# Kernel tuning notes

Measured on AMD Instinct MI355X. Metric: run time of the kernel, lower is better.

Reference implementation:

```python
import jax, jax.numpy as jnp
import numpy as np

N = 8192
IN_F = 256
OUT_F = 256


def setup_inputs() -> dict:
    key = jax.random.key(0)
    k_v, k_adj, k1, k2, k3, kb = jax.random.split(key, 6)
    stdv = 1.0 / np.sqrt(OUT_F)
    V = jax.random.normal(k_v, (N, IN_F), dtype=jnp.float32)
    adj = jax.random.randint(k_adj, (N, N), 0, 4, dtype=jnp.int32)
    w1 = jax.random.uniform(k1, (IN_F, OUT_F), jnp.float32, -stdv, stdv)
    w2 = jax.random.uniform(k2, (IN_F, OUT_F), jnp.float32, -stdv, stdv)
    w3 = jax.random.uniform(k3, (IN_F, OUT_F), jnp.float32, -stdv, stdv)
    bias = jax.random.uniform(kb, (OUT_F,), jnp.float32, -stdv, stdv)
    return {"V": V, "adj": adj, "w1": w1, "w2": w2, "w3": w3, "bias": bias}


def reference(V, adj, w1, w2, w3, bias):
    # typed relational GCN: for each edge type k in {1,2,3},
    # aggregate (adj==k) @ (V @ wk), then sum and add bias
    o1 = jnp.matmul((adj == 1).astype(jnp.float32), jnp.matmul(V, w1))
    o2 = jnp.matmul((adj == 2).astype(jnp.float32), jnp.matmul(V, w2))
    o3 = jnp.matmul((adj == 3).astype(jnp.float32), jnp.matmul(V, w3))
    return o1 + o2 + o3 + bias
```

## Files before the change

kernel.cpp:

```cpp
#include <hip/hip_runtime.h>

typedef __attribute__((ext_vector_type(4))) float f32x4;
typedef __attribute__((ext_vector_type(16))) float f32x16;
typedef __attribute__((ext_vector_type(4))) unsigned short u16x4;
typedef __attribute__((ext_vector_type(4))) int i32x4;
typedef __attribute__((ext_vector_type(8))) __bf16 bf16x8;

union FragAB {
  u16x4 u[2];
  i32x4 v;
  bf16x8 f;
};

static __device__ __forceinline__ unsigned short f2bf(float x) {
  union { float f; unsigned u; } v;
  v.f = x;
  unsigned r = v.u + 0x7FFFu + ((v.u >> 16) & 1u);
  return (unsigned short)(r >> 16);
}

#define NN 8192

__global__ __launch_bounds__(256) void k_bias(const float* __restrict__ bias,
                                              float* __restrict__ out) {
  out[(size_t)blockIdx.x * 256 + threadIdx.x] = bias[threadIdx.x];
}

__global__ __launch_bounds__(256) void k_transform(
    const float* __restrict__ V, const float* __restrict__ w1,
    const float* __restrict__ w2, const float* __restrict__ w3,
    unsigned short* __restrict__ Bp) {
  int bx = blockIdx.x;
  int rb = bx & 63;
  int nb = bx >> 6;
  const float* W = (nb < 4) ? w1 : (nb < 8) ? w2 : w3;
  int nc0 = (nb & 3) * 64;
  int tid = threadIdx.x;
  int lane = tid & 63;
  int wv = tid >> 6;
  int wm = wv >> 1, wn = wv & 1;
  int q = lane >> 4, l16 = lane & 15;

  __shared__ unsigned short tA[128][36];
  __shared__ unsigned short tB[64][36];

  f32x4 acc[4][2];
#pragma unroll
  for (int i = 0; i < 4; i++)
#pragma unroll
    for (int j = 0; j < 2; j++) acc[i][j] = (f32x4)0.0f;

  for (int kk = 0; kk < 256; kk += 32) {
    {
      int r = tid >> 1, c0 = (tid & 1) * 16;
      const float* src = V + (size_t)(rb * 128 + r) * 256 + kk + c0;
      f32x4 f0 = *(const f32x4*)(src + 0);
      f32x4 f1 = *(const f32x4*)(src + 4);
      f32x4 f2 = *(const f32x4*)(src + 8);
      f32x4 f3 = *(const f32x4*)(src + 12);
      unsigned short* d = &tA[r][c0];
      d[0] = f2bf(f0.x);  d[1] = f2bf(f0.y);  d[2] = f2bf(f0.z);  d[3] = f2bf(f0.w);
      d[4] = f2bf(f1.x);  d[5] = f2bf(f1.y);  d[6] = f2bf(f1.z);  d[7] = f2bf(f1.w);
      d[8] = f2bf(f2.x);  d[9] = f2bf(f2.y);  d[10] = f2bf(f2.z); d[11] = f2bf(f2.w);
      d[12] = f2bf(f3.x); d[13] = f2bf(f3.y); d[14] = f2bf(f3.z); d[15] = f2bf(f3.w);
    }
    {
      int r = tid >> 3, c0 = (tid & 7) * 8;
      const float* src = W + (size_t)(kk + r) * 256 + nc0 + c0;
      f32x4 g0 = *(const f32x4*)(src);
      f32x4 g1 = *(const f32x4*)(src + 4);
      tB[c0 + 0][r] = f2bf(g0.x); tB[c0 + 1][r] = f2bf(g0.y);
      tB[c0 + 2][r] = f2bf(g0.z); tB[c0 + 3][r] = f2bf(g0.w);
      tB[c0 + 4][r] = f2bf(g1.x); tB[c0 + 5][r] = f2bf(g1.y);
      tB[c0 + 6][r] = f2bf(g1.z); tB[c0 + 7][r] = f2bf(g1.w);
    }
    __syncthreads();
    FragAB af[4], bf[2];
#pragma unroll
    for (int mt = 0; mt < 4; mt++) {
      const unsigned short* p = &tA[wm * 64 + mt * 16 + l16][q * 8];
      af[mt].u[0] = *(const u16x4*)p;
      af[mt].u[1] = *(const u16x4*)(p + 4);
    }
#pragma unroll
    for (int nt = 0; nt < 2; nt++) {
      const unsigned short* p = &tB[wn * 32 + nt * 16 + l16][q * 8];
      bf[nt].u[0] = *(const u16x4*)p;
      bf[nt].u[1] = *(const u16x4*)(p + 4);
    }
#pragma unroll
    for (int mt = 0; mt < 4; mt++)
#pragma unroll
      for (int nt = 0; nt < 2; nt++)
        acc[mt][nt] = __builtin_amdgcn_mfma_f32_16x16x32_bf16(
            af[mt].f, bf[nt].f, acc[mt][nt], 0, 0, 0);
    __syncthreads();
  }
  int ty = nb >> 2;
#pragma unroll
  for (int mt = 0; mt < 4; mt++)
#pragma unroll
    for (int nt = 0; nt < 2; nt++) {
      int n = (nb & 3) * 64 + wn * 32 + nt * 16 + l16;
      int j0 = rb * 128 + wm * 64 + mt * 16 + q * 4;
      u16x4 hv;
      hv.x = f2bf(acc[mt][nt].x);
      hv.y = f2bf(acc[mt][nt].y);
      hv.z = f2bf(acc[mt][nt].z);
      hv.w = f2bf(acc[mt][nt].w);
      size_t idx = (size_t)ty * 2097152 + (size_t)(j0 >> 4) * 4096 + n * 16 + (j0 & 15);
      *(u16x4*)(Bp + idx) = hv;
    }
}

__global__ __launch_bounds__(512) void k_agg(const int* __restrict__ adj,
                                             const unsigned short* __restrict__ Bp,
                                             float* __restrict__ out) {
  int bx = blockIdx.x;
  int ks = bx & 3, rb = bx >> 2;
  int tid = threadIdx.x, lane = tid & 63;
  int wv = tid >> 6;
  int wm = wv >> 2, wn = wv & 3;
  int q = lane >> 5, l32 = lane & 31;

  __shared__ unsigned short msk[3][128][36];

  f32x16 acc[2][2];
  acc[0][0] = (f32x16)0.0f;
  acc[0][1] = (f32x16)0.0f;
  acc[1][0] = (f32x16)0.0f;
  acc[1][1] = (f32x16)0.0f;

  int sr = tid >> 2, scg = tid & 3;
  const int* ap = adj + (size_t)(rb * 128 + sr) * NN + ks * 2048 + scg * 8;

  const unsigned short* bb[3][2];
#pragma unroll
  for (int ty = 0; ty < 3; ty++)
#pragma unroll
    for (int nt = 0; nt < 2; nt++) {
      int n = wn * 64 + nt * 32 + l32;
      bb[ty][nt] = Bp + (size_t)ty * 2097152 + (size_t)ks * 524288 + n * 16 + q * 8;
    }

  i32x4 a0 = *(const i32x4*)ap;
  i32x4 a1 = *(const i32x4*)(ap + 4);

  for (int step = 0; step < 64; step++) {
    {
      int av[8] = {a0.x, a0.y, a0.z, a0.w, a1.x, a1.y, a1.z, a1.w};
#pragma unroll
      for (int ty = 0; ty < 3; ty++) {
        u16x4 lo, hi;
        lo.x = (av[0] == ty + 1) ? 0x3F80 : 0;
        lo.y = (av[1] == ty + 1) ? 0x3F80 : 0;
        lo.z = (av[2] == ty + 1) ? 0x3F80 : 0;
        lo.w = (av[3] == ty + 1) ? 0x3F80 : 0;
        hi.x = (av[4] == ty + 1) ? 0x3F80 : 0;
        hi.y = (av[5] == ty + 1) ? 0x3F80 : 0;
        hi.z = (av[6] == ty + 1) ? 0x3F80 : 0;
        hi.w = (av[7] == ty + 1) ? 0x3F80 : 0;
        unsigned short* d = &msk[ty][sr][scg * 8];
        *(u16x4*)d = lo;
        *(u16x4*)(d + 4) = hi;
      }
    }
    __syncthreads();
    if (step < 63) {
      ap += 32;
      a0 = *(const i32x4*)ap;
      a1 = *(const i32x4*)(ap + 4);
    }
    int boff = step * 8192;
#pragma unroll
    for (int kh = 0; kh < 2; kh++)
#pragma unroll
      for (int ty = 0; ty < 3; ty++) {
        FragAB af[2], bf[2];
#pragma unroll
        for (int mt = 0; mt < 2; mt++) {
          const unsigned short* p =
              &msk[ty][wm * 64 + mt * 32 + l32][kh * 16 + q * 8];
          af[mt].u[0] = *(const u16x4*)p;
          af[mt].u[1] = *(const u16x4*)(p + 4);
        }
#pragma unroll
        for (int nt = 0; nt < 2; nt++) {
          const unsigned short* p = bb[ty][nt] + boff + kh * 4096;
          bf[nt].v = *(const i32x4*)p;
        }
        acc[0][0] = __builtin_amdgcn_mfma_f32_32x32x16_bf16(af[0].f, bf[0].f,
                                                            acc[0][0], 0, 0, 0);
        acc[0][1] = __builtin_amdgcn_mfma_f32_32x32x16_bf16(af[0].f, bf[1].f,
                                                            acc[0][1], 0, 0, 0);
        acc[1][0] = __builtin_amdgcn_mfma_f32_32x32x16_bf16(af[1].f, bf[0].f,
                                                            acc[1][0], 0, 0, 0);
        acc[1][1] = __builtin_amdgcn_mfma_f32_32x32x16_bf16(af[1].f, bf[1].f,
                                                            acc[1][1], 0, 0, 0);
      }
    __syncthreads();
  }
#pragma unroll
  for (int mt = 0; mt < 2; mt++)
#pragma unroll
    for (int nt = 0; nt < 2; nt++) {
      int colbase = wn * 64 + nt * 32 + l32;
      int rowb = rb * 128 + wm * 64 + mt * 32 + 4 * q;
#pragma unroll
      for (int r = 0; r < 16; r++) {
        int row = rowb + (r & 3) + 8 * (r >> 2);
        atomicAdd(out + (size_t)row * 256 + colbase, acc[mt][nt][r]);
      }
    }
}

extern "C" void kernel_launch(void* const* d_in, const int* in_sizes, int n_in,
                              void* d_out, int out_size, void* d_ws,
                              size_t ws_size, hipStream_t stream) {
  const float* V = (const float*)d_in[0];
  const int* adj = (const int*)d_in[1];
  const float* w1 = (const float*)d_in[2];
  const float* w2 = (const float*)d_in[3];
  const float* w3 = (const float*)d_in[4];
  const float* bias = (const float*)d_in[5];
  float* out = (float*)d_out;
  unsigned short* Bp = (unsigned short*)d_ws;

  k_bias<<<dim3(NN), dim3(256), 0, stream>>>(bias, out);
  k_transform<<<dim3(768), dim3(256), 0, stream>>>(V, w1, w2, w3, Bp);
  k_agg<<<dim3(256), dim3(512), 0, stream>>>(adj, Bp, out);
}
```

Measured before the change: 577.5 us.

## Double-buffer adjacency masks and retile aggregation into smaller blocks with more K-splits

Result: faster. 488.3 us (-15.4%).

```diff
diff --git a/kernel.cpp b/kernel.cpp
--- a/kernel.cpp
+++ b/kernel.cpp
@@ -113,17 +113,16 @@
     }
 }
 
-__global__ __launch_bounds__(512) void k_agg(const int* __restrict__ adj,
+__global__ __launch_bounds__(256) void k_agg(const int* __restrict__ adj,
                                              const unsigned short* __restrict__ Bp,
                                              float* __restrict__ out) {
   int bx = blockIdx.x;
-  int ks = bx & 3, rb = bx >> 2;
+  int ks = bx & 7, rb = bx >> 3;
   int tid = threadIdx.x, lane = tid & 63;
-  int wv = tid >> 6;
-  int wm = wv >> 2, wn = wv & 3;
+  int wn = tid >> 6;
   int q = lane >> 5, l32 = lane & 31;
 
-  __shared__ unsigned short msk[3][128][36];
+  __shared__ unsigned short msk[2][3][64][36];
 
   f32x16 acc[2][2];
   acc[0][0] = (f32x16)0.0f;
@@ -132,7 +131,7 @@
   acc[1][1] = (f32x16)0.0f;
 
   int sr = tid >> 2, scg = tid & 3;
-  const int* ap = adj + (size_t)(rb * 128 + sr) * NN + ks * 2048 + scg * 8;
+  const int* ap = adj + (size_t)(rb * 64 + sr) * NN + ks * 1024 + scg * 8;
 
   const unsigned short* bb[3][2];
 #pragma unroll
@@ -140,14 +139,71 @@
 #pragma unroll
     for (int nt = 0; nt < 2; nt++) {
       int n = wn * 64 + nt * 32 + l32;
-      bb[ty][nt] = Bp + (size_t)ty * 2097152 + (size_t)ks * 524288 + n * 16 + q * 8;
+      bb[ty][nt] = Bp + (size_t)ty * 2097152 + (size_t)ks * 262144 + n * 16 + q * 8;
     }
 
   i32x4 a0 = *(const i32x4*)ap;
   i32x4 a1 = *(const i32x4*)(ap + 4);
-
-  for (int step = 0; step < 64; step++) {
-    {
+  ap += 32;
+  {
+    int av[8] = {a0.x, a0.y, a0.z, a0.w, a1.x, a1.y, a1.z, a1.w};
+#pragma unroll
+    for (int ty = 0; ty < 3; ty++) {
+      u16x4 lo, hi;
+      lo.x = (av[0] == ty + 1) ? 0x3F80 : 0;
+      lo.y = (av[1] == ty + 1) ? 0x3F80 : 0;
+      lo.z = (av[2] == ty + 1) ? 0x3F80 : 0;
+      lo.w = (av[3] == ty + 1) ? 0x3F80 : 0;
+      hi.x = (av[4] == ty + 1) ? 0x3F80 : 0;
+      hi.y = (av[5] == ty + 1) ? 0x3F80 : 0;
+      hi.z = (av[6] == ty + 1) ? 0x3F80 : 0;
+      hi.w = (av[7] == ty + 1) ? 0x3F80 : 0;
+      unsigned short* d = &msk[0][ty][sr][scg * 8];
+      *(u16x4*)d = lo;
+      *(u16x4*)(d + 4) = hi;
+    }
+  }
+  a0 = *(const i32x4*)ap;
+  a1 = *(const i32x4*)(ap + 4);
+  ap += 32;
+  __syncthreads();
+
+  for (int step = 0; step < 32; step++) {
+    int buf = step & 1;
+    FragAB bv[2][3][2];
+    size_t soff = (size_t)step * 8192;
+#pragma unroll
+    for (int kh = 0; kh < 2; kh++)
+#pragma unroll
+      for (int ty = 0; ty < 3; ty++)
+#pragma unroll
+        for (int nt = 0; nt < 2; nt++)
+          bv[kh][ty][nt].v = *(const i32x4*)(bb[ty][nt] + soff + kh * 4096);
+    FragAB af[2][3][2];
+#pragma unroll
+    for (int kh = 0; kh < 2; kh++)
+#pragma unroll
+      for (int ty = 0; ty < 3; ty++)
+#pragma unroll
+        for (int mt = 0; mt < 2; mt++) {
+          const unsigned short* p = &msk[buf][ty][mt * 32 + l32][kh * 16 + q * 8];
+          af[kh][ty][mt].u[0] = *(const u16x4*)p;
+          af[kh][ty][mt].u[1] = *(const u16x4*)(p + 4);
+        }
+#pragma unroll
+    for (int kh = 0; kh < 2; kh++)
+#pragma unroll
+      for (int ty = 0; ty < 3; ty++) {
+        acc[0][0] = __builtin_amdgcn_mfma_f32_32x32x16_bf16(
+            af[kh][ty][0].f, bv[kh][ty][0].f, acc[0][0], 0, 0, 0);
+        acc[0][1] = __builtin_amdgcn_mfma_f32_32x32x16_bf16(
+            af[kh][ty][0].f, bv[kh][ty][1].f, acc[0][1], 0, 0, 0);
+        acc[1][0] = __builtin_amdgcn_mfma_f32_32x32x16_bf16(
+            af[kh][ty][1].f, bv[kh][ty][0].f, acc[1][0], 0, 0, 0);
+        acc[1][1] = __builtin_amdgcn_mfma_f32_32x32x16_bf16(
+            af[kh][ty][1].f, bv[kh][ty][1].f, acc[1][1], 0, 0, 0);
+      }
+    if (step < 31) {
       int av[8] = {a0.x, a0.y, a0.z, a0.w, a1.x, a1.y, a1.z, a1.w};
 #pragma unroll
       for (int ty = 0; ty < 3; ty++) {
@@ -160,44 +216,16 @@
         hi.y = (av[5] == ty + 1) ? 0x3F80 : 0;
         hi.z = (av[6] == ty + 1) ? 0x3F80 : 0;
         hi.w = (av[7] == ty + 1) ? 0x3F80 : 0;
-        unsigned short* d = &msk[ty][sr][scg * 8];
+        unsigned short* d = &msk[buf ^ 1][ty][sr][scg * 8];
         *(u16x4*)d = lo;
         *(u16x4*)(d + 4) = hi;
       }
-    }
-    __syncthreads();
-    if (step < 63) {
-      ap += 32;
-      a0 = *(const i32x4*)ap;
-      a1 = *(const i32x4*)(ap + 4);
-    }
-    int boff = step * 8192;
-#pragma unroll
-    for (int kh = 0; kh < 2; kh++)
-#pragma unroll
-      for (int ty = 0; ty < 3; ty++) {
-        FragAB af[2], bf[2];
-#pragma unroll
-        for (int mt = 0; mt < 2; mt++) {
-          const unsigned short* p =
-              &msk[ty][wm * 64 + mt * 32 + l32][kh * 16 + q * 8];
-          af[mt].u[0] = *(const u16x4*)p;
-          af[mt].u[1] = *(const u16x4*)(p + 4);
-        }
-#pragma unroll
-        for (int nt = 0; nt < 2; nt++) {
-          const unsigned short* p = bb[ty][nt] + boff + kh * 4096;
-          bf[nt].v = *(const i32x4*)p;
-        }
-        acc[0][0] = __builtin_amdgcn_mfma_f32_32x32x16_bf16(af[0].f, bf[0].f,
-                                                            acc[0][0], 0, 0, 0);
-        acc[0][1] = __builtin_amdgcn_mfma_f32_32x32x16_bf16(af[0].f, bf[1].f,
-                                                            acc[0][1], 0, 0, 0);
-        acc[1][0] = __builtin_amdgcn_mfma_f32_32x32x16_bf16(af[1].f, bf[0].f,
-                                                            acc[1][0], 0, 0, 0);
-        acc[1][1] = __builtin_amdgcn_mfma_f32_32x32x16_bf16(af[1].f, bf[1].f,
-                                                            acc[1][1], 0, 0, 0);
-      }
+      if (step < 30) {
+        a0 = *(const i32x4*)ap;
+        a1 = *(const i32x4*)(ap + 4);
+        ap += 32;
+      }
+    }
     __syncthreads();
   }
 #pragma unroll
@@ -205,7 +233,7 @@
 #pragma unroll
     for (int nt = 0; nt < 2; nt++) {
       int colbase = wn * 64 + nt * 32 + l32;
-      int rowb = rb * 128 + wm * 64 + mt * 32 + 4 * q;
+      int rowb = rb * 64 + mt * 32 + 4 * q;
 #pragma unroll
       for (int r = 0; r < 16; r++) {
         int row = rowb + (r & 3) + 8 * (r >> 2);
@@ -228,5 +256,5 @@
 
   k_bias<<<dim3(NN), dim3(256), 0, stream>>>(bias, out);
   k_transform<<<dim3(768), dim3(256), 0, stream>>>(V, w1, w2, w3, Bp);
-  k_agg<<<dim3(256), dim3(512), 0, stream>>>(adj, Bp, out);
-}
+  k_agg<<<dim3(1024), dim3(256), 0, stream>>>(adj, Bp, out);
+}
```

## Restructure aggregation kernel with per-wave private adj staging and no block barriers

Applied to the files above, without the earlier changes.

Result: faster. 490.0 us (-15.2%).

```diff
diff --git a/kernel.cpp b/kernel.cpp
--- a/kernel.cpp
+++ b/kernel.cpp
@@ -113,17 +113,17 @@
     }
 }
 
-__global__ __launch_bounds__(512) void k_agg(const int* __restrict__ adj,
+__global__ __launch_bounds__(256) void k_agg(const int* __restrict__ adj,
                                              const unsigned short* __restrict__ Bp,
                                              float* __restrict__ out) {
   int bx = blockIdx.x;
   int ks = bx & 3, rb = bx >> 2;
   int tid = threadIdx.x, lane = tid & 63;
   int wv = tid >> 6;
-  int wm = wv >> 2, wn = wv & 3;
   int q = lane >> 5, l32 = lane & 31;
 
-  __shared__ unsigned short msk[3][128][36];
+  __shared__ __align__(16) int smem[16384];
+  int* wbase = smem + wv * 4096;
 
   f32x16 acc[2][2];
   acc[0][0] = (f32x16)0.0f;
@@ -131,81 +131,90 @@
   acc[1][0] = (f32x16)0.0f;
   acc[1][1] = (f32x16)0.0f;
 
-  int sr = tid >> 2, scg = tid & 3;
-  const int* ap = adj + (size_t)(rb * 128 + sr) * NN + ks * 2048 + scg * 8;
+  const int* ast = adj + (size_t)(rb * 64 + (lane >> 3)) * NN + ks * 2048 + (lane & 7) * 4;
+  int swzw = (((lane & 7) ^ ((lane >> 3) & 7)) * 4);
+  int wrow = (lane >> 3) * 32;
+  int sw7 = l32 & 7;
 
   const unsigned short* bb[3][2];
 #pragma unroll
   for (int ty = 0; ty < 3; ty++)
 #pragma unroll
     for (int nt = 0; nt < 2; nt++) {
-      int n = wn * 64 + nt * 32 + l32;
+      int n = wv * 64 + nt * 32 + l32;
       bb[ty][nt] = Bp + (size_t)ty * 2097152 + (size_t)ks * 524288 + n * 16 + q * 8;
     }
 
-  i32x4 a0 = *(const i32x4*)ap;
-  i32x4 a1 = *(const i32x4*)(ap + 4);
-
-  for (int step = 0; step < 64; step++) {
-    {
-      int av[8] = {a0.x, a0.y, a0.z, a0.w, a1.x, a1.y, a1.z, a1.w};
-#pragma unroll
-      for (int ty = 0; ty < 3; ty++) {
-        u16x4 lo, hi;
-        lo.x = (av[0] == ty + 1) ? 0x3F80 : 0;
-        lo.y = (av[1] == ty + 1) ? 0x3F80 : 0;
-        lo.z = (av[2] == ty + 1) ? 0x3F80 : 0;
-        lo.w = (av[3] == ty + 1) ? 0x3F80 : 0;
-        hi.x = (av[4] == ty + 1) ? 0x3F80 : 0;
-        hi.y = (av[5] == ty + 1) ? 0x3F80 : 0;
-        hi.z = (av[6] == ty + 1) ? 0x3F80 : 0;
-        hi.w = (av[7] == ty + 1) ? 0x3F80 : 0;
-        unsigned short* d = &msk[ty][sr][scg * 8];
-        *(u16x4*)d = lo;
-        *(u16x4*)(d + 4) = hi;
+  i32x4 st[8];
+#pragma unroll
+  for (int j = 0; j < 8; j++) st[j] = *(const i32x4*)(ast + j * 8 * NN);
+#pragma unroll
+  for (int j = 0; j < 8; j++)
+    *(i32x4*)(wbase + j * 256 + wrow + swzw) = st[j];
+#pragma unroll
+  for (int j = 0; j < 8; j++) st[j] = *(const i32x4*)(ast + j * 8 * NN + 32);
+
+  for (int s = 0; s < 64; s++) {
+    int bufoff = (s & 1) * 2048;
+    FragAB bv[2][3][2];
+    size_t soff = (size_t)s * 8192;
+#pragma unroll
+    for (int kh = 0; kh < 2; kh++)
+#pragma unroll
+      for (int ty = 0; ty < 3; ty++)
+#pragma unroll
+        for (int nt = 0; nt < 2; nt++)
+          bv[kh][ty][nt].v = *(const i32x4*)(bb[ty][nt] + soff + kh * 4096);
+
+#pragma unroll
+    for (int kh = 0; kh < 2; kh++)
+#pragma unroll
+      for (int mt = 0; mt < 2; mt++) {
+        int rowoff = bufoff + mt * 1024 + l32 * 32;
+        int c0 = kh * 4 + q * 2;
+        i32x4 e0 = *(const i32x4*)(wbase + rowoff + ((c0 ^ sw7) * 4));
+        i32x4 e1 = *(const i32x4*)(wbase + rowoff + (((c0 + 1) ^ sw7) * 4));
+#pragma unroll
+        for (int ty = 0; ty < 3; ty++) {
+          FragAB af;
+          u16x4 lo, hi;
+          int t = ty + 1;
+          lo.x = (e0.x == t) ? 0x3F80 : 0;
+          lo.y = (e0.y == t) ? 0x3F80 : 0;
+          lo.z = (e0.z == t) ? 0x3F80 : 0;
+          lo.w = (e0.w == t) ? 0x3F80 : 0;
+          hi.x = (e1.x == t) ? 0x3F80 : 0;
+          hi.y = (e1.y == t) ? 0x3F80 : 0;
+          hi.z = (e1.z == t) ? 0x3F80 : 0;
+          hi.w = (e1.w == t) ? 0x3F80 : 0;
+          af.u[0] = lo;
+          af.u[1] = hi;
+          acc[mt][0] = __builtin_amdgcn_mfma_f32_32x32x16_bf16(
+              af.f, bv[kh][ty][0].f, acc[mt][0], 0, 0, 0);
+          acc[mt][1] = __builtin_amdgcn_mfma_f32_32x32x16_bf16(
+              af.f, bv[kh][ty][1].f, acc[mt][1], 0, 0, 0);
+        }
       }
-    }
-    __syncthreads();
-    if (step < 63) {
-      ap += 32;
-      a0 = *(const i32x4*)ap;
-      a1 = *(const i32x4*)(ap + 4);
-    }
-    int boff = step * 8192;
-#pragma unroll
-    for (int kh = 0; kh < 2; kh++)
-#pragma unroll
-      for (int ty = 0; ty < 3; ty++) {
-        FragAB af[2], bf[2];
-#pragma unroll
-        for (int mt = 0; mt < 2; mt++) {
-          const unsigned short* p =
-              &msk[ty][wm * 64 + mt * 32 + l32][kh * 16 + q * 8];
-          af[mt].u[0] = *(const u16x4*)p;
-          af[mt].u[1] = *(const u16x4*)(p + 4);
-        }
-#pragma unroll
-        for (int nt = 0; nt < 2; nt++) {
-          const unsigned short* p = bb[ty][nt] + boff + kh * 4096;
-          bf[nt].v = *(const i32x4*)p;
-        }
-        acc[0][0] = __builtin_amdgcn_mfma_f32_32x32x16_bf16(af[0].f, bf[0].f,
-                                                            acc[0][0], 0, 0, 0);
-        acc[0][1] = __builtin_amdgcn_mfma_f32_32x32x16_bf16(af[0].f, bf[1].f,
-                                                            acc[0][1], 0, 0, 0);
-        acc[1][0] = __builtin_amdgcn_mfma_f32_32x32x16_bf16(af[1].f, bf[0].f,
-                                                            acc[1][0], 0, 0, 0);
-        acc[1][1] = __builtin_amdgcn_mfma_f32_32x32x16_bf16(af[1].f, bf[1].f,
-                                                            acc[1][1], 0, 0, 0);
+
+    if (s < 63) {
+      int obuf = bufoff ^ 2048;
+#pragma unroll
+      for (int j = 0; j < 8; j++)
+        *(i32x4*)(wbase + obuf + j * 256 + wrow + swzw) = st[j];
+      if (s < 62) {
+        const int* anext = ast + (s + 2) * 32;
+#pragma unroll
+        for (int j = 0; j < 8; j++) st[j] = *(const i32x4*)(anext + j * 8 * NN);
       }
-    __syncthreads();
+    }
   }
+
 #pragma unroll
   for (int mt = 0; mt < 2; mt++)
 #pragma unroll
     for (int nt = 0; nt < 2; nt++) {
-      int colbase = wn * 64 + nt * 32 + l32;
-      int rowb = rb * 128 + wm * 64 + mt * 32 + 4 * q;
+      int colbase = wv * 64 + nt * 32 + l32;
+      int rowb = rb * 64 + mt * 32 + 4 * q;
 #pragma unroll
       for (int r = 0; r < 16; r++) {
         int row = rowb + (r & 3) + 8 * (r >> 2);
@@ -228,5 +237,5 @@
 
   k_bias<<<dim3(NN), dim3(256), 0, stream>>>(bias, out);
   k_transform<<<dim3(768), dim3(256), 0, stream>>>(V, w1, w2, w3, Bp);
-  k_agg<<<dim3(256), dim3(512), 0, stream>>>(adj, Bp, out);
-}
+  k_agg<<<dim3(512), dim3(256), 0, stream>>>(adj, Bp, out);
+}
```
